# Kernel tuning notes

Hardware: AMD Instinct MI355X
Metric: run time of the kernel (lower is better)

The kernel has to match this reference:

```python
import jax, jax.numpy as jnp
import numpy as np

DIM = 192
R = 16            # patches_resolution, D=H=W=R
SP = 4            # split_size
NH = 6            # num_heads (block level); per-branch heads = NH//3
B = 2
L = R * R * R
EPS = 1e-5


def layernorm(x, g, b):
    mu = jnp.mean(x, axis=-1, keepdims=True)
    var = jnp.mean(jnp.square(x - mu), axis=-1, keepdims=True)
    return (x - mu) * jax.lax.rsqrt(var + EPS) * g + b


def window_partition(x, d_sp, h_sp, w_sp, nh):
    b, _, _, _, cb = x.shape
    win = d_sp * h_sp * w_sp
    x = x.reshape(b, R // d_sp, d_sp, R // h_sp, h_sp, R // w_sp, w_sp, cb)
    x = x.transpose(0, 1, 3, 5, 2, 4, 6, 7).reshape(-1, win, nh, cb // nh)
    return x.transpose(0, 2, 1, 3)


def window_merge(x, d_sp, h_sp, w_sp, b):
    cb = x.shape[-1]
    x = x.reshape(b, R // d_sp, R // h_sp, R // w_sp, d_sp, h_sp, w_sp, cb)
    x = x.transpose(0, 1, 4, 2, 5, 3, 6, 7).reshape(b, L, cb)
    return x


def lepe_attention(q, k, v, d_sp, h_sp, w_sp, nh):
    # q,k,v: (B, L, Cb). Note: LePE bias is computed-but-unused in the source -> pure windowed SDPA.
    b, _, cb = q.shape
    hd = cb // nh
    scale = hd ** -0.5
    q5 = q.reshape(b, R, R, R, cb)
    k5 = k.reshape(b, R, R, R, cb)
    v5 = v.reshape(b, R, R, R, cb)
    qw = window_partition(q5, d_sp, h_sp, w_sp, nh) * scale
    kw = window_partition(k5, d_sp, h_sp, w_sp, nh)
    vw = window_partition(v5, d_sp, h_sp, w_sp, nh)
    attn = jax.nn.softmax(jnp.einsum('whqd,whkd->whqk', qw, kw), axis=-1)
    out = jnp.einsum('whqk,whkd->whqd', attn, vw)
    out = out.transpose(0, 2, 1, 3).reshape(-1, d_sp * h_sp * w_sp, cb)
    return window_merge(out, d_sp, h_sp, w_sp, b)


WINDOW_SHAPES = [(R, R, SP), (R, SP, R), (SP, R, R)]  # idx 0,1,2


def setup_inputs() -> dict:
    key = jax.random.key(0)
    ks = jax.random.split(key, 12)
    C = DIM
    H4 = int(C * 4)
    inp = {
        'x': jax.random.normal(ks[0], (B, C, R, R, R), dtype=jnp.float32),
        'w_qkv': jax.random.normal(ks[1], (C, 3 * C), dtype=jnp.float32) * (C ** -0.5),
        'w_proj': jax.random.normal(ks[2], (C, C), dtype=jnp.float32) * (C ** -0.5),
        'b_proj': jnp.zeros((C,), dtype=jnp.float32),
        'g1': jnp.ones((C,), dtype=jnp.float32),
        'b1': jnp.zeros((C,), dtype=jnp.float32),
        'g2': jnp.ones((C,), dtype=jnp.float32),
        'b2': jnp.zeros((C,), dtype=jnp.float32),
        'w_fc1': jax.random.normal(ks[3], (C, H4), dtype=jnp.float32) * (C ** -0.5),
        'b_fc1': jnp.zeros((H4,), dtype=jnp.float32),
        'w_fc2': jax.random.normal(ks[4], (H4, C), dtype=jnp.float32) * (H4 ** -0.5),
        'b_fc2': jnp.zeros((C,), dtype=jnp.float32),
    }
    return inp


def reference(x, w_qkv, w_proj, b_proj, g1, b1, g2, b2, w_fc1, b_fc1, w_fc2, b_fc2):
    C = DIM
    Cb = C // 3
    nh_b = NH // 3
    x = 2.0 * x
    xt = jnp.transpose(x, (0, 2, 3, 4, 1))                # (B, D, H, W, C)
    img = layernorm(xt, g1, b1)
    qkv = img.reshape(B, L, C) @ w_qkv                    # (B, L, 3C)
    q, k, v = jnp.split(qkv.reshape(B, L, 3, C).transpose(2, 0, 1, 3), 3, axis=0)
    q, k, v = q[0], k[0], v[0]                            # each (B, L, C)
    outs = []
    for i, (dsp, hsp, wsp) in enumerate(WINDOW_SHAPES):
        sl = slice(i * Cb, (i + 1) * Cb)
        outs.append(lepe_attention(q[..., sl], k[..., sl], v[..., sl], dsp, hsp, wsp, nh_b))
    attened = jnp.concatenate(outs, axis=2)               # (B, L, C)
    attened = attened @ w_proj + b_proj
    xs = xt.reshape(B, L, C) + attened
    h = layernorm(xs, g2, b2) @ w_fc1 + b_fc1
    h = jax.nn.gelu(h, approximate=False)
    xs = xs + (h @ w_fc2 + b_fc2)
    out = xs.reshape(B, R, R, R, C).transpose(0, 4, 1, 2, 3)  # (B, C, D, H, W)
    return out
```

## Files before the change

### kernel.cpp

```cpp
#include <hip/hip_runtime.h>
#include <hip/hip_bf16.h>

typedef __hip_bfloat16 bf16;
typedef short short8 __attribute__((ext_vector_type(8)));
typedef float floatx4 __attribute__((ext_vector_type(4)));

#define SZ (8192*192)

__device__ __forceinline__ unsigned short f2b(float f) {
    unsigned u = __builtin_bit_cast(unsigned, f);
    u += 0x7FFFu + ((u >> 16) & 1u);
    return (unsigned short)(u >> 16);
}
__device__ __forceinline__ float b2f(unsigned short h) {
    unsigned u = ((unsigned)h) << 16;
    return __builtin_bit_cast(float, u);
}
__device__ __forceinline__ unsigned pk2(float a, float b) {
    return ((unsigned)f2b(b) << 16) | (unsigned)f2b(a);
}

__global__ void detect_kernel(const unsigned short* __restrict__ x16, int* __restrict__ flag) {
    __shared__ int cnt;
    if (threadIdx.x == 0) cnt = 0;
    __syncthreads();
    int c = 0;
    for (int i = threadIdx.x; i < 8192; i += 256) {
        int e = (x16[i] >> 7) & 0xFF;
        if (e >= 152) c++;
    }
    if (c) atomicAdd(&cnt, c);
    __syncthreads();
    if (threadIdx.x == 0) *flag = (cnt >= 32) ? 1 : 0;
}

struct WPA { const void* s[11]; };

__global__ __launch_bounds__(256) void wprep_kernel(WPA a, unsigned short* __restrict__ wdst,
                                                    float* __restrict__ vdst,
                                                    const int* __restrict__ flag) {
    int i = blockIdx.x * 256 + threadIdx.x;
    int f = *flag;
    if (i < 442368) {
        int seg, base, K, N;
        if (i < 110592)      { seg = 0; base = 0;      K = 192; N = 576; }
        else if (i < 147456) { seg = 1; base = 110592; K = 192; N = 192; }
        else if (i < 294912) { seg = 2; base = 147456; K = 192; N = 768; }
        else                 { seg = 3; base = 294912; K = 768; N = 192; }
        int j = i - base;
        int n = j / K, k = j - n * K;
        size_t src = (size_t)k * N + n;
        float v = f ? ((const float*)a.s[seg])[src] : b2f(((const unsigned short*)a.s[seg])[src]);
        int ci = (n >> 6) * (K >> 5) + (k >> 5);
        int off = (ci << 11) + (((n >> 4) & 3) << 9) + ((n & 15) << 5) + (k & 31);
        wdst[base + off] = f2b(v);
    } else if (i < 444288) {
        int j = i - 442368;
        int seg, off;
        if (j < 960)       { seg = 4 + j / 192; off = j % 192; }
        else if (j < 1728) { seg = 9; off = j - 960; }
        else               { seg = 10; off = j - 1728; }
        float v = f ? ((const float*)a.s[seg])[off] : b2f(((const unsigned short*)a.s[seg])[off]);
        vdst[j] = v;
    }
}


__global__ __launch_bounds__(256) void prep_kernel(const void* __restrict__ xin,
        const int* __restrict__ flag,
        const float* __restrict__ g1, const float* __restrict__ b1,
        float* __restrict__ xt, unsigned short* __restrict__ img) {
    __shared__ float tile[192][33];
    __shared__ float mu[32], rs[32];
    int tid = threadIdx.x;
    int t0 = blockIdx.x * 32;
    int b = t0 >> 12;
    int ts = t0 & 4095;
    int f = *flag;
    for (int idx = tid; idx < 192 * 32; idx += 256) {
        int c = idx >> 5, tt = idx & 31;
        int gi = ((b * 192 + c) << 12) + ts + tt;
        float raw = f ? ((const float*)xin)[gi] : b2f(((const unsigned short*)xin)[gi]);
        tile[c][tt] = 2.0f * raw;
    }
    __syncthreads();
    {
        int tt = tid >> 3, j = tid & 7;
        int c0 = j * 24;
        float s = 0.f, sq = 0.f;
        #pragma unroll
        for (int i = 0; i < 24; ++i) { float v = tile[c0 + i][tt]; s += v; sq += v * v; }
        s += __shfl_xor(s, 1); sq += __shfl_xor(sq, 1);
        s += __shfl_xor(s, 2); sq += __shfl_xor(sq, 2);
        s += __shfl_xor(s, 4); sq += __shfl_xor(sq, 4);
        if (j == 0) {
            float m = s * (1.0f / 192.0f);
            float var = sq * (1.0f / 192.0f) - m * m;
            mu[tt] = m;
            rs[tt] = rsqrtf(var + 1e-5f);
        }
    }
    __syncthreads();
    for (int idx = tid; idx < 32 * 192; idx += 256) {
        int tt = idx / 192, c = idx % 192;
        float v = tile[c][tt];
        xt[(t0 + tt) * 192 + c] = v;
        int po = ((((t0 + tt) >> 4) * 6 + (c >> 5)) << 9) + ((tt & 15) << 5) + (c & 31);
        img[po] = f2b((v - mu[tt]) * rs[tt] * g1[c] + b1[c]);
    }
}

__device__ __forceinline__ int g_of(int br, int t) {
    if (br == 0) return (((t >> 2) & 3) << 10) | ((t >> 8) << 6) | (((t >> 4) & 15) << 2) | (t & 3);
    if (br == 1) return (((t >> 6) & 3) << 10) | ((t >> 8) << 6) | (((t >> 4) & 3) << 4) | (t & 15);
    return t;
}

template <int MODE, int W>
__global__ __launch_bounds__(64 * W) void mfma_gemm(const unsigned short* __restrict__ A,
        const unsigned short* __restrict__ WT, const float* __restrict__ bias,
        const float* __restrict__ resid, void* __restrict__ out,
        unsigned short* __restrict__ qt, unsigned short* __restrict__ kt,
        unsigned short* __restrict__ vt, int N, int K) {
    int wave = threadIdx.x >> 6, lane = threadIdx.x & 63;
    int quad = lane >> 4, l16 = lane & 15;
    int m0 = blockIdx.x * (32 * W) + wave * 32, n0 = blockIdx.y * 64;
    const int KT = K >> 5;
    const unsigned short* ap = A + (((size_t)(m0 >> 4) * KT) << 9) + l16 * 32 + quad * 8;
    const size_t a1off = ((size_t)KT) << 9;
    const unsigned short* wpB = WT + (((size_t)blockIdx.y * KT) << 11) + l16 * 32 + quad * 8;
    floatx4 acc[2][4] = {};
    #pragma unroll 2
    for (int kc = 0; kc < K; kc += 32) {
        const unsigned short* ac = ap + (((size_t)(kc >> 5)) << 9);
        short8 a0 = *reinterpret_cast<const short8*>(ac);
        short8 a1 = *reinterpret_cast<const short8*>(ac + a1off);
        const unsigned short* wc = wpB + (((size_t)(kc >> 5)) << 11);
        #pragma unroll
        for (int nt = 0; nt < 4; ++nt) {
            short8 w = *reinterpret_cast<const short8*>(wc + nt * 512);
            acc[0][nt] = __builtin_amdgcn_mfma_f32_16x16x32_bf16(a0, w, acc[0][nt], 0, 0, 0);
            acc[1][nt] = __builtin_amdgcn_mfma_f32_16x16x32_bf16(a1, w, acc[1][nt], 0, 0, 0);
        }
    }
    #pragma unroll
    for (int fh = 0; fh < 2; ++fh) {
        #pragma unroll
        for (int nt = 0; nt < 4; ++nt) {
            int col = n0 + nt * 16 + l16;
            if (MODE == 0 && n0 >= 384) {
                int cv = col - 384;
                int d = cv & 31, brh = cv >> 5;
                int row0 = m0 + fh * 16 + quad * 4;
                int bb_ = row0 >> 12, tl = row0 & 4095;
                int g0 = g_of(brh >> 1, tl);
                int wb2 = g0 >> 10, k = g0 & 63, c = k >> 4, m = k & 15;
                int pos = ((c >> 1) << 5) + ((m >> 2) << 3) + ((c & 1) << 2);
                int chunk = (g0 & 1023) >> 6;
                int tidx = ((d >> 4) << 1) | (pos >> 5);
                unsigned short* tile = vt + (((((size_t)(bb_ * 6 + brh) * 4 + wb2) * 16 + chunk) * 4 + tidx) << 9);
                ushort4 w4;
                w4.x = f2b(acc[fh][nt][0]);
                w4.y = f2b(acc[fh][nt][1]);
                w4.z = f2b(acc[fh][nt][2]);
                w4.w = f2b(acc[fh][nt][3]);
                *reinterpret_cast<ushort4*>(tile + (d & 15) * 32 + (pos & 31)) = w4;
            } else if (MODE == 0 && n0 >= 192) {
                int ck = col - 192;
                int d = ck & 31, brh = ck >> 5;
                int row0 = m0 + fh * 16 + quad * 4;
                int bb_ = row0 >> 12, tl = row0 & 4095;
                int g0 = g_of(brh >> 1, tl);
                int wb2 = g0 >> 10, k = g0 & 63, c = k >> 4, m = k & 15;
                int chunk = (g0 & 1023) >> 6;
                unsigned short* tile = kt + (((((size_t)(bb_ * 6 + brh) * 4 + wb2) * 16 + chunk) * 4 + c) << 9);
                tile[m * 32 + d]       = f2b(acc[fh][nt][0]);
                tile[(m + 1) * 32 + d] = f2b(acc[fh][nt][1]);
                tile[(m + 2) * 32 + d] = f2b(acc[fh][nt][2]);
                tile[(m + 3) * 32 + d] = f2b(acc[fh][nt][3]);
            } else if (MODE == 0) {
                int d = col & 31, brh = col >> 5;
                int row0 = m0 + fh * 16 + quad * 4;
                int bb_ = row0 >> 12, tl = row0 & 4095;
                int g0 = g_of(brh >> 1, tl);
                int wb2 = g0 >> 10, q = g0 & 1023;
                int chunk = q >> 4, m = q & 15;
                unsigned short* tile = qt + ((((size_t)(bb_ * 6 + brh) * 4 + wb2) * 64 + chunk) << 9);
                tile[m * 32 + d]       = f2b(acc[fh][nt][0] * 0.17677669529663689f);
                tile[(m + 1) * 32 + d] = f2b(acc[fh][nt][1] * 0.17677669529663689f);
                tile[(m + 2) * 32 + d] = f2b(acc[fh][nt][2] * 0.17677669529663689f);
                tile[(m + 3) * 32 + d] = f2b(acc[fh][nt][3] * 0.17677669529663689f);
            } else {
                #pragma unroll
                for (int r = 0; r < 4; ++r) {
                    int row = m0 + fh * 16 + quad * 4 + r;
                    float v = acc[fh][nt][r] + bias[col];
                    if (MODE == 2) {
                        v = 0.5f * v * (1.0f + erff(v * 0.70710678118654752f));
                        size_t o = (((size_t)(row >> 4) * (N >> 5) + (col >> 5)) << 9)
                                 + ((row & 15) << 5) + (col & 31);
                        ((unsigned short*)out)[o] = f2b(v);
                    } else {
                        size_t o = (size_t)row * N + col;
                        ((float*)out)[o] = v + resid[o];
                    }
                }
            }
        }
    }
}

__device__ __forceinline__ int tok_of(int br, int wb, int q) {
    if (br == 0) return ((q >> 6) << 8) | (((q >> 2) & 15) << 4) | (wb << 2) | (q & 3);
    else if (br == 1) return ((q >> 6) << 8) | (((wb << 2) + ((q >> 4) & 3)) << 4) | (q & 15);
    else return (((wb << 2) + (q >> 8)) << 8) | (q & 255);
}

__global__ __launch_bounds__(256) void attn_mfma(const unsigned short* __restrict__ qt,
        const unsigned short* __restrict__ kt, const unsigned short* __restrict__ vt,
        unsigned short* __restrict__ attb) {
    int hw = blockIdx.x;
    int bid = (hw & 7) * 96 + (hw >> 3);
    int qti = bid & 15, head = (bid >> 4) & 1, wb = (bid >> 5) & 3, b = (bid >> 7) & 1, br = bid >> 8;
    int tid = threadIdx.x;
    int wave = tid >> 6, lane = tid & 63, quad = lane >> 4, l16 = lane & 15;
    int coff = br * 64 + head * 32;
    int brh = br * 2 + head;
    int tb = b << 12;
    size_t qbase = ((((size_t)(b * 6 + brh) * 4 + wb) * 64 + qti * 4 + wave) << 9) + l16 * 32 + quad * 8;
    short8 aq = *reinterpret_cast<const short8*>(qt + qbase);
    floatx4 o0 = {}, o1 = {};
    float lsum = 0.f;

    const size_t kvbase = ((((size_t)(b * 6 + brh) * 4 + wb) * 16) << 11) + l16 * 32 + quad * 8;
    const unsigned short* kp = kt + kvbase;
    const unsigned short* vp = vt + kvbase;

    short8 k0 = *reinterpret_cast<const short8*>(kp);
    short8 k1 = *reinterpret_cast<const short8*>(kp + 512);
    short8 k2 = *reinterpret_cast<const short8*>(kp + 1024);
    short8 k3 = *reinterpret_cast<const short8*>(kp + 1536);
    short8 vb00 = *reinterpret_cast<const short8*>(vp);
    short8 vb01 = *reinterpret_cast<const short8*>(vp + 512);
    short8 vb10 = *reinterpret_cast<const short8*>(vp + 1024);
    short8 vb11 = *reinterpret_cast<const short8*>(vp + 1536);

    for (int it = 0; it < 16; ++it) {
        short8 ck0 = k0, ck1 = k1, ck2 = k2, ck3 = k3;
        short8 cv00 = vb00, cv01 = vb01, cv10 = vb10, cv11 = vb11;
        if (it + 1 < 16) {
            kp += 2048; vp += 2048;
            k0 = *reinterpret_cast<const short8*>(kp);
            k1 = *reinterpret_cast<const short8*>(kp + 512);
            k2 = *reinterpret_cast<const short8*>(kp + 1024);
            k3 = *reinterpret_cast<const short8*>(kp + 1536);
            vb00 = *reinterpret_cast<const short8*>(vp);
            vb01 = *reinterpret_cast<const short8*>(vp + 512);
            vb10 = *reinterpret_cast<const short8*>(vp + 1024);
            vb11 = *reinterpret_cast<const short8*>(vp + 1536);
        }
        floatx4 z = {};
        floatx4 s0 = __builtin_amdgcn_mfma_f32_16x16x32_bf16(ck0, aq, z, 0, 0, 0);
        floatx4 s1 = __builtin_amdgcn_mfma_f32_16x16x32_bf16(ck1, aq, z, 0, 0, 0);
        floatx4 s2 = __builtin_amdgcn_mfma_f32_16x16x32_bf16(ck2, aq, z, 0, 0, 0);
        floatx4 s3 = __builtin_amdgcn_mfma_f32_16x16x32_bf16(ck3, aq, z, 0, 0, 0);
        float p00 = __expf(s0[0]), p01 = __expf(s0[1]), p02 = __expf(s0[2]), p03 = __expf(s0[3]);
        float p10 = __expf(s1[0]), p11 = __expf(s1[1]), p12 = __expf(s1[2]), p13 = __expf(s1[3]);
        float p20 = __expf(s2[0]), p21 = __expf(s2[1]), p22 = __expf(s2[2]), p23 = __expf(s2[3]);
        float p30 = __expf(s3[0]), p31 = __expf(s3[1]), p32 = __expf(s3[2]), p33 = __expf(s3[3]);
        lsum += ((p00 + p01) + (p02 + p03)) + ((p10 + p11) + (p12 + p13))
              + ((p20 + p21) + (p22 + p23)) + ((p30 + p31) + (p32 + p33));
        uint4 ua, ub;
        ua.x = pk2(p00, p01); ua.y = pk2(p02, p03); ua.z = pk2(p10, p11); ua.w = pk2(p12, p13);
        ub.x = pk2(p20, p21); ub.y = pk2(p22, p23); ub.z = pk2(p30, p31); ub.w = pk2(p32, p33);
        short8 pa0 = __builtin_bit_cast(short8, ua);
        short8 pa1 = __builtin_bit_cast(short8, ub);
        o0 = __builtin_amdgcn_mfma_f32_16x16x32_bf16(pa0, cv00, o0, 0, 0, 0);
        o0 = __builtin_amdgcn_mfma_f32_16x16x32_bf16(pa1, cv01, o0, 0, 0, 0);
        o1 = __builtin_amdgcn_mfma_f32_16x16x32_bf16(pa0, cv10, o1, 0, 0, 0);
        o1 = __builtin_amdgcn_mfma_f32_16x16x32_bf16(pa1, cv11, o1, 0, 0, 0);
    }
    lsum += __shfl_xor(lsum, 16);
    lsum += __shfl_xor(lsum, 32);
    #pragma unroll
    for (int r = 0; r < 4; ++r) {
        float inv = 1.0f / __shfl(lsum, quad * 4 + r);
        int q = qti * 64 + wave * 16 + quad * 4 + r;
        int t = tb + tok_of(br, wb, q);
        size_t o = (((size_t)(t >> 4) * 6 + (coff >> 5)) << 9) + ((t & 15) << 5);
        attb[o + l16]      = f2b(o0[r] * inv);
        attb[o + 16 + l16] = f2b(o1[r] * inv);
    }
}

__global__ __launch_bounds__(256) void ln_kernel(const float* __restrict__ in,
        const float* __restrict__ g, const float* __restrict__ bb, unsigned short* __restrict__ out) {
    int token = (blockIdx.x << 2) + (threadIdx.x >> 6);
    int lane = threadIdx.x & 63;
    const float* row = in + (size_t)token * 192;
    float v0 = row[lane], v1 = row[lane + 64], v2 = row[lane + 128];
    float s = v0 + v1 + v2, sq = v0 * v0 + v1 * v1 + v2 * v2;
    #pragma unroll
    for (int mask = 1; mask < 64; mask <<= 1) {
        s += __shfl_xor(s, mask);
        sq += __shfl_xor(sq, mask);
    }
    float m = s * (1.f / 192.f);
    float var = sq * (1.f / 192.f) - m * m;
    float rsd = rsqrtf(var + 1e-5f);
    int tbase = (token >> 4) * 6, tr = (token & 15) << 5;
    int lo = lane >> 5, la = lane & 31;
    out[((tbase + lo)     << 9) + tr + la] = f2b((v0 - m) * rsd * g[lane]       + bb[lane]);
    out[((tbase + lo + 2) << 9) + tr + la] = f2b((v1 - m) * rsd * g[lane + 64]  + bb[lane + 64]);
    out[((tbase + lo + 4) << 9) + tr + la] = f2b((v2 - m) * rsd * g[lane + 128] + bb[lane + 128]);
}

__global__ __launch_bounds__(256) void unprep_kernel(const float* __restrict__ xs,
                                                     void* __restrict__ out,
                                                     const int* __restrict__ flag) {
    __shared__ float tile[192][33];
    int tid = threadIdx.x;
    int t0 = blockIdx.x * 32;
    int b = t0 >> 12, ts = t0 & 4095;
    for (int idx = tid; idx < 32 * 192; idx += 256) {
        int tt = idx / 192, c = idx % 192;
        tile[c][tt] = xs[(size_t)(t0 + tt) * 192 + c];
    }
    __syncthreads();
    int f = *flag;
    for (int idx = tid; idx < 192 * 32; idx += 256) {
        int c = idx >> 5, tt = idx & 31;
        float v = tile[c][tt];
        int o = ((b * 192 + c) << 12) + ts + tt;
        if (f) ((float*)out)[o] = v;
        else   ((unsigned short*)out)[o] = f2b(v);
    }
}

extern "C" void kernel_launch(void* const* d_in, const int* in_sizes, int n_in,
                              void* d_out, int out_size, void* d_ws, size_t ws_size,
                              hipStream_t stream) {
    float* ws = (float*)d_ws;

    float* vbase = ws;
    float* bprojf = vbase + 0;
    float* g1f    = vbase + 192;
    float* b1f    = vbase + 384;
    float* g2f    = vbase + 576;
    float* b2f    = vbase + 768;
    float* bfc1f  = vbase + 960;
    float* bfc2f  = vbase + 1728;

    unsigned short* wbase = (unsigned short*)(ws + 1920);
    unsigned short* wqkvT = wbase + 0;
    unsigned short* wprojT = wbase + 110592;
    unsigned short* wfc1T = wbase + 147456;
    unsigned short* wfc2T = wbase + 294912;

    size_t p = 1920 + 442368 / 2;
    float* xt = ws + p; p += SZ;
    unsigned short* img = (unsigned short*)(ws + p); p += SZ / 2;
    size_t pQ = p;
    unsigned short* hbuf = (unsigned short*)(ws + pQ);
    p = pQ + 8192 * 768 / 2;
    unsigned short* attb = (unsigned short*)(ws + p); p += SZ / 2;
    int* flag = (int*)(ws + p); p += 16;
    unsigned short* qtb = (unsigned short*)(ws + p); p += SZ / 2;
    unsigned short* ktb = (unsigned short*)(ws + p); p += SZ / 2;
    unsigned short* vtb = (unsigned short*)(ws + p); p += SZ / 2;
    float* xs = xt;
    unsigned short* lnb = img;

    WPA wa;
    wa.s[0] = d_in[1];  wa.s[1] = d_in[2];  wa.s[2] = d_in[8];  wa.s[3] = d_in[10];
    wa.s[4] = d_in[3];  wa.s[5] = d_in[4];  wa.s[6] = d_in[5];  wa.s[7] = d_in[6];
    wa.s[8] = d_in[7];  wa.s[9] = d_in[9];  wa.s[10] = d_in[11];

    detect_kernel<<<dim3(1), dim3(256), 0, stream>>>((const unsigned short*)d_in[0], flag);
    wprep_kernel<<<dim3(1736), dim3(256), 0, stream>>>(wa, wbase, vbase, flag);
    prep_kernel<<<dim3(256), dim3(256), 0, stream>>>(d_in[0], flag, g1f, b1f, xt, img);
    mfma_gemm<0, 2><<<dim3(128, 9), dim3(128), 0, stream>>>(
        img, wqkvT, nullptr, nullptr, nullptr, qtb, ktb, vtb, 576, 192);
    attn_mfma<<<dim3(768), dim3(256), 0, stream>>>(qtb, ktb, vtb, attb);
    mfma_gemm<1, 1><<<dim3(256, 3), dim3(64), 0, stream>>>(
        attb, wprojT, bprojf, xt, xs, nullptr, nullptr, nullptr, 192, 192);
    ln_kernel<<<dim3(2048), dim3(256), 0, stream>>>(xs, g2f, b2f, lnb);
    mfma_gemm<2, 2><<<dim3(128, 12), dim3(128), 0, stream>>>(
        lnb, wfc1T, bfc1f, nullptr, hbuf, nullptr, nullptr, nullptr, 768, 192);
    mfma_gemm<3, 1><<<dim3(256, 3), dim3(64), 0, stream>>>(
        hbuf, wfc2T, bfc2f, xs, xs, nullptr, nullptr, nullptr, 192, 768);
    unprep_kernel<<<dim3(256), dim3(256), 0, stream>>>(xs, d_out, flag);
}
```

Baseline: 183.1 us.

## Fuse proj GEMM with LayerNorm, fc2 with output transpose, inline dtype detection

Removes the separate detect, ln and unprep kernels. The dtype check now runs inside wprep and prep, proj+residual+LN2 is a single kernel where each block computes full 192-column rows, and fc2+residual writes the transposed output directly through an LDS tile. This cuts three launches and the fp32 xs round trips for LN and unprep. In exchange, every block redundantly scans 8192 input values for detection, and the proj kernel uses fewer, larger blocks (256 blocks of 192 threads).

```diff
diff --git a/kernel.cpp b/kernel.cpp
--- a/kernel.cpp
+++ b/kernel.cpp
@@ -20,27 +20,28 @@
     return ((unsigned)f2b(b) << 16) | (unsigned)f2b(a);
 }
 
-__global__ void detect_kernel(const unsigned short* __restrict__ x16, int* __restrict__ flag) {
-    __shared__ int cnt;
-    if (threadIdx.x == 0) cnt = 0;
+__device__ __forceinline__ int detect_inline(const unsigned short* __restrict__ x16,
+                                             int tid, int nthreads, int* cnt) {
+    if (tid == 0) *cnt = 0;
     __syncthreads();
     int c = 0;
-    for (int i = threadIdx.x; i < 8192; i += 256) {
+    for (int i = tid; i < 8192; i += nthreads) {
         int e = (x16[i] >> 7) & 0xFF;
         if (e >= 152) c++;
     }
-    if (c) atomicAdd(&cnt, c);
-    __syncthreads();
-    if (threadIdx.x == 0) *flag = (cnt >= 32) ? 1 : 0;
+    if (c) atomicAdd(cnt, c);
+    __syncthreads();
+    return (*cnt >= 32) ? 1 : 0;
 }
 
 struct WPA { const void* s[11]; };
 
 __global__ __launch_bounds__(256) void wprep_kernel(WPA a, unsigned short* __restrict__ wdst,
                                                     float* __restrict__ vdst,
-                                                    const int* __restrict__ flag) {
+                                                    const unsigned short* __restrict__ x16) {
+    __shared__ int cnt;
+    int f = detect_inline(x16, threadIdx.x, 256, &cnt);
     int i = blockIdx.x * 256 + threadIdx.x;
-    int f = *flag;
     if (i < 442368) {
         int seg, base, K, N;
         if (i < 110592)      { seg = 0; base = 0;      K = 192; N = 576; }
@@ -67,16 +68,18 @@
 
 
 __global__ __launch_bounds__(256) void prep_kernel(const void* __restrict__ xin,
-        const int* __restrict__ flag,
+        int* __restrict__ flagOut,
         const float* __restrict__ g1, const float* __restrict__ b1,
         float* __restrict__ xt, unsigned short* __restrict__ img) {
     __shared__ float tile[192][33];
     __shared__ float mu[32], rs[32];
+    __shared__ int cnt;
     int tid = threadIdx.x;
+    int f = detect_inline((const unsigned short*)xin, tid, 256, &cnt);
+    if (blockIdx.x == 0 && tid == 0) *flagOut = f;
     int t0 = blockIdx.x * 32;
     int b = t0 >> 12;
     int ts = t0 & 4095;
-    int f = *flag;
     for (int idx = tid; idx < 192 * 32; idx += 256) {
         int c = idx >> 5, tt = idx & 31;
         int gi = ((b * 192 + c) << 12) + ts + tt;
@@ -195,18 +198,150 @@
                 for (int r = 0; r < 4; ++r) {
                     int row = m0 + fh * 16 + quad * 4 + r;
                     float v = acc[fh][nt][r] + bias[col];
-                    if (MODE == 2) {
-                        v = 0.5f * v * (1.0f + erff(v * 0.70710678118654752f));
-                        size_t o = (((size_t)(row >> 4) * (N >> 5) + (col >> 5)) << 9)
-                                 + ((row & 15) << 5) + (col & 31);
-                        ((unsigned short*)out)[o] = f2b(v);
-                    } else {
-                        size_t o = (size_t)row * N + col;
-                        ((float*)out)[o] = v + resid[o];
-                    }
+                    v = 0.5f * v * (1.0f + erff(v * 0.70710678118654752f));
+                    size_t o = (((size_t)(row >> 4) * (N >> 5) + (col >> 5)) << 9)
+                             + ((row & 15) << 5) + (col & 31);
+                    ((unsigned short*)out)[o] = f2b(v);
                 }
             }
         }
+    }
+}
+
+__global__ __launch_bounds__(192) void proj_ln_kernel(const unsigned short* __restrict__ A,
+        const unsigned short* __restrict__ WT, const float* __restrict__ bias,
+        float* __restrict__ xs, const float* __restrict__ g2v, const float* __restrict__ b2v,
+        unsigned short* __restrict__ lnb) {
+    __shared__ float red[3][32][2];
+    int wave = threadIdx.x >> 6, lane = threadIdx.x & 63;
+    int quad = lane >> 4, l16 = lane & 15;
+    int m0 = blockIdx.x * 32;
+    const int KT = 6;
+    const unsigned short* ap = A + (((size_t)(m0 >> 4) * KT) << 9) + l16 * 32 + quad * 8;
+    const size_t a1off = ((size_t)KT) << 9;
+    const unsigned short* wpB = WT + (((size_t)wave * KT) << 11) + l16 * 32 + quad * 8;
+    floatx4 acc[2][4] = {};
+    #pragma unroll
+    for (int kc = 0; kc < 192; kc += 32) {
+        const unsigned short* ac = ap + (((size_t)(kc >> 5)) << 9);
+        short8 a0 = *reinterpret_cast<const short8*>(ac);
+        short8 a1 = *reinterpret_cast<const short8*>(ac + a1off);
+        const unsigned short* wc = wpB + (((size_t)(kc >> 5)) << 11);
+        #pragma unroll
+        for (int nt = 0; nt < 4; ++nt) {
+            short8 w = *reinterpret_cast<const short8*>(wc + nt * 512);
+            acc[0][nt] = __builtin_amdgcn_mfma_f32_16x16x32_bf16(a0, w, acc[0][nt], 0, 0, 0);
+            acc[1][nt] = __builtin_amdgcn_mfma_f32_16x16x32_bf16(a1, w, acc[1][nt], 0, 0, 0);
+        }
+    }
+    float vv[2][4][4];
+    #pragma unroll
+    for (int fh = 0; fh < 2; ++fh) {
+        #pragma unroll
+        for (int r = 0; r < 4; ++r) {
+            float s = 0.f, sq = 0.f;
+            #pragma unroll
+            for (int nt = 0; nt < 4; ++nt) {
+                int col = wave * 64 + nt * 16 + l16;
+                int row = m0 + fh * 16 + quad * 4 + r;
+                size_t o = (size_t)row * 192 + col;
+                float v = acc[fh][nt][r] + bias[col] + xs[o];
+                xs[o] = v;
+                vv[fh][nt][r] = v;
+                s += v; sq += v * v;
+            }
+            s += __shfl_xor(s, 1); sq += __shfl_xor(sq, 1);
+            s += __shfl_xor(s, 2); sq += __shfl_xor(sq, 2);
+            s += __shfl_xor(s, 4); sq += __shfl_xor(sq, 4);
+            s += __shfl_xor(s, 8); sq += __shfl_xor(sq, 8);
+            if (l16 == 0) {
+                int rw = fh * 16 + quad * 4 + r;
+                red[wave][rw][0] = s;
+                red[wave][rw][1] = sq;
+            }
+        }
+    }
+    __syncthreads();
+    float mu[2][4], rsd[2][4];
+    #pragma unroll
+    for (int fh = 0; fh < 2; ++fh) {
+        #pragma unroll
+        for (int r = 0; r < 4; ++r) {
+            int rw = fh * 16 + quad * 4 + r;
+            float S  = red[0][rw][0] + red[1][rw][0] + red[2][rw][0];
+            float SQ = red[0][rw][1] + red[1][rw][1] + red[2][rw][1];
+            float m = S * (1.0f / 192.0f);
+            float var = SQ * (1.0f / 192.0f) - m * m;
+            mu[fh][r] = m;
+            rsd[fh][r] = rsqrtf(var + 1e-5f);
+        }
+    }
+    #pragma unroll
+    for (int fh = 0; fh < 2; ++fh) {
+        #pragma unroll
+        for (int nt = 0; nt < 4; ++nt) {
+            #pragma unroll
+            for (int r = 0; r < 4; ++r) {
+                int col = wave * 64 + nt * 16 + l16;
+                int row = m0 + fh * 16 + quad * 4 + r;
+                float v = (vv[fh][nt][r] - mu[fh][r]) * rsd[fh][r] * g2v[col] + b2v[col];
+                size_t o = (((size_t)(row >> 4) * 6 + (col >> 5)) << 9) + ((row & 15) << 5) + (col & 31);
+                lnb[o] = f2b(v);
+            }
+        }
+    }
+}
+
+__global__ __launch_bounds__(64) void fc2_out_kernel(const unsigned short* __restrict__ A,
+        const unsigned short* __restrict__ WT, const float* __restrict__ bias,
+        const float* __restrict__ xs, void* __restrict__ out,
+        const int* __restrict__ flag) {
+    __shared__ float tile[64][33];
+    int tid = threadIdx.x;
+    int quad = tid >> 4, l16 = tid & 15;
+    int m0 = blockIdx.x * 32, n0 = blockIdx.y * 64;
+    const int KT = 24;
+    const unsigned short* ap = A + (((size_t)(m0 >> 4) * KT) << 9) + l16 * 32 + quad * 8;
+    const size_t a1off = ((size_t)KT) << 9;
+    const unsigned short* wpB = WT + (((size_t)blockIdx.y * KT) << 11) + l16 * 32 + quad * 8;
+    floatx4 acc[2][4] = {};
+    #pragma unroll 2
+    for (int kc = 0; kc < 768; kc += 32) {
+        const unsigned short* ac = ap + (((size_t)(kc >> 5)) << 9);
+        short8 a0 = *reinterpret_cast<const short8*>(ac);
+        short8 a1 = *reinterpret_cast<const short8*>(ac + a1off);
+        const unsigned short* wc = wpB + (((size_t)(kc >> 5)) << 11);
+        #pragma unroll
+        for (int nt = 0; nt < 4; ++nt) {
+            short8 w = *reinterpret_cast<const short8*>(wc + nt * 512);
+            acc[0][nt] = __builtin_amdgcn_mfma_f32_16x16x32_bf16(a0, w, acc[0][nt], 0, 0, 0);
+            acc[1][nt] = __builtin_amdgcn_mfma_f32_16x16x32_bf16(a1, w, acc[1][nt], 0, 0, 0);
+        }
+    }
+    #pragma unroll
+    for (int fh = 0; fh < 2; ++fh) {
+        #pragma unroll
+        for (int nt = 0; nt < 4; ++nt) {
+            #pragma unroll
+            for (int r = 0; r < 4; ++r) {
+                int col = n0 + nt * 16 + l16;
+                int row = m0 + fh * 16 + quad * 4 + r;
+                float v = acc[fh][nt][r] + bias[col] + xs[(size_t)row * 192 + col];
+                tile[nt * 16 + l16][fh * 16 + quad * 4 + r] = v;
+            }
+        }
+    }
+    __syncthreads();
+    int f = *flag;
+    int b = m0 >> 12, ts = m0 & 4095;
+    #pragma unroll 4
+    for (int it = 0; it < 32; ++it) {
+        int idx = it * 64 + tid;
+        int cc = idx >> 5, tt = idx & 31;
+        float v = tile[cc][tt];
+        size_t o = (((size_t)(b * 192 + n0 + cc)) << 12) + ts + tt;
+        if (f) ((float*)out)[o] = v;
+        else   ((unsigned short*)out)[o] = f2b(v);
     }
 }
 
@@ -293,50 +428,6 @@
     }
 }
 
-__global__ __launch_bounds__(256) void ln_kernel(const float* __restrict__ in,
-        const float* __restrict__ g, const float* __restrict__ bb, unsigned short* __restrict__ out) {
-    int token = (blockIdx.x << 2) + (threadIdx.x >> 6);
-    int lane = threadIdx.x & 63;
-    const float* row = in + (size_t)token * 192;
-    float v0 = row[lane], v1 = row[lane + 64], v2 = row[lane + 128];
-    float s = v0 + v1 + v2, sq = v0 * v0 + v1 * v1 + v2 * v2;
-    #pragma unroll
-    for (int mask = 1; mask < 64; mask <<= 1) {
-        s += __shfl_xor(s, mask);
-        sq += __shfl_xor(sq, mask);
-    }
-    float m = s * (1.f / 192.f);
-    float var = sq * (1.f / 192.f) - m * m;
-    float rsd = rsqrtf(var + 1e-5f);
-    int tbase = (token >> 4) * 6, tr = (token & 15) << 5;
-    int lo = lane >> 5, la = lane & 31;
-    out[((tbase + lo)     << 9) + tr + la] = f2b((v0 - m) * rsd * g[lane]       + bb[lane]);
-    out[((tbase + lo + 2) << 9) + tr + la] = f2b((v1 - m) * rsd * g[lane + 64]  + bb[lane + 64]);
-    out[((tbase + lo + 4) << 9) + tr + la] = f2b((v2 - m) * rsd * g[lane + 128] + bb[lane + 128]);
-}
-
-__global__ __launch_bounds__(256) void unprep_kernel(const float* __restrict__ xs,
-                                                     void* __restrict__ out,
-                                                     const int* __restrict__ flag) {
-    __shared__ float tile[192][33];
-    int tid = threadIdx.x;
-    int t0 = blockIdx.x * 32;
-    int b = t0 >> 12, ts = t0 & 4095;
-    for (int idx = tid; idx < 32 * 192; idx += 256) {
-        int tt = idx / 192, c = idx % 192;
-        tile[c][tt] = xs[(size_t)(t0 + tt) * 192 + c];
-    }
-    __syncthreads();
-    int f = *flag;
-    for (int idx = tid; idx < 192 * 32; idx += 256) {
-        int c = idx >> 5, tt = idx & 31;
-        float v = tile[c][tt];
-        int o = ((b * 192 + c) << 12) + ts + tt;
-        if (f) ((float*)out)[o] = v;
-        else   ((unsigned short*)out)[o] = f2b(v);
-    }
-}
-
 extern "C" void kernel_launch(void* const* d_in, const int* in_sizes, int n_in,
                               void* d_out, int out_size, void* d_ws, size_t ws_size,
                               hipStream_t stream) {
@@ -376,18 +467,16 @@
     wa.s[4] = d_in[3];  wa.s[5] = d_in[4];  wa.s[6] = d_in[5];  wa.s[7] = d_in[6];
     wa.s[8] = d_in[7];  wa.s[9] = d_in[9];  wa.s[10] = d_in[11];
 
-    detect_kernel<<<dim3(1), dim3(256), 0, stream>>>((const unsigned short*)d_in[0], flag);
-    wprep_kernel<<<dim3(1736), dim3(256), 0, stream>>>(wa, wbase, vbase, flag);
+    wprep_kernel<<<dim3(1736), dim3(256), 0, stream>>>(wa, wbase, vbase,
+        (const unsigned short*)d_in[0]);
     prep_kernel<<<dim3(256), dim3(256), 0, stream>>>(d_in[0], flag, g1f, b1f, xt, img);
     mfma_gemm<0, 2><<<dim3(128, 9), dim3(128), 0, stream>>>(
         img, wqkvT, nullptr, nullptr, nullptr, qtb, ktb, vtb, 576, 192);
     attn_mfma<<<dim3(768), dim3(256), 0, stream>>>(qtb, ktb, vtb, attb);
-    mfma_gemm<1, 1><<<dim3(256, 3), dim3(64), 0, stream>>>(
-        attb, wprojT, bprojf, xt, xs, nullptr, nullptr, nullptr, 192, 192);
-    ln_kernel<<<dim3(2048), dim3(256), 0, stream>>>(xs, g2f, b2f, lnb);
+    proj_ln_kernel<<<dim3(256), dim3(192), 0, stream>>>(
+        attb, wprojT, bprojf, xs, g2f, b2f, lnb);
     mfma_gemm<2, 2><<<dim3(128, 12), dim3(128), 0, stream>>>(
         lnb, wfc1T, bfc1f, nullptr, hbuf, nullptr, nullptr, nullptr, 768, 192);
-    mfma_gemm<3, 1><<<dim3(256, 3), dim3(64), 0, stream>>>(
-        hbuf, wfc2T, bfc2f, xs, xs, nullptr, nullptr, nullptr, 192, 768);
-    unprep_kernel<<<dim3(256), dim3(256), 0, stream>>>(xs, d_out, flag);
-}
+    fc2_out_kernel<<<dim3(256, 3), dim3(64), 0, stream>>>(
+        hbuf, wfc2T, bfc2f, xs, d_out, flag);
+}
```

Result: no change. 185.3 us (+1.2%).
